# Optimization experiments

Measured on AMD Instinct MI355X. Metric: run time of the kernel, lower is better.

The kernel has to match this reference:

```python
import jax, jax.numpy as jnp
import numpy as np

B, N1, K, E, H = 64, 8, 128, 256, 512


def setup_inputs() -> dict:
    key = jax.random.key(0)
    ks = jax.random.split(key, 10)
    s = 1.0 / np.sqrt(E)
    sh = 1.0 / np.sqrt(H)
    return {
        "queries": jax.random.normal(ks[0], (B, N1, E), jnp.float32),
        "keys": jax.random.normal(ks[1], (B, N1, K, E), jnp.float32),
        "cum_subs_masks": jax.random.randint(ks[2], (B, N1, K, 1), 0, 2, jnp.int32),
        "num_neg": N1 - 1,
        "wk_w": jax.random.uniform(ks[3], (H, E), jnp.float32, -s, s),
        "wk_b": jax.random.uniform(ks[4], (H,), jnp.float32, -s, s),
        "wq_w": jax.random.uniform(ks[5], (H, E), jnp.float32, -s, s),
        "wq_b": jax.random.uniform(ks[6], (H,), jnp.float32, -s, s),
        "wv_w": jax.random.uniform(ks[7], (1, H), jnp.float32, -sh, sh),
        "wv_b": jax.random.uniform(ks[8], (1,), jnp.float32, -sh, sh),
    }


def reference(queries, keys, cum_subs_masks, num_neg, wk_w, wk_b, wq_w, wq_b, wv_w, wv_b):
    # queries: (B, N1, E) -> project and broadcast over keys dim
    q_proj = jnp.einsum("bne,he->bnh", queries, wq_w) + wq_b        # (B, N1, H)
    k_proj = jnp.einsum("bnke,he->bnkh", keys, wk_w) + wk_b          # (B, N1, K, H)
    hidden = jnp.tanh(q_proj[:, :, None, :] + k_proj)                # (B, N1, K, H)
    scores = jnp.einsum("bnkh,oh->bnko", hidden, wv_w) + wv_b        # (B, N1, K, 1)
    scores = scores + cum_subs_masks.astype(scores.dtype) * (-1e9)
    attn_weight = jax.nn.softmax(scores, axis=-2)                    # over K
    attn_out = jnp.sum(attn_weight * keys, axis=-2)                  # (B, N1, E)
    return attn_out, attn_weight
```

## Files before the change

### kernel.cpp

```cpp
#include <hip/hip_runtime.h>
#include <hip/hip_bf16.h>

#define B_  64
#define N1_ 8
#define KK  128
#define EE  256
#define HH  512
#define BN  (B_ * N1_)

typedef __attribute__((ext_vector_type(8))) short short8;
typedef __attribute__((ext_vector_type(4))) float f32x4;

__device__ __forceinline__ short bfs(float f) {
  __hip_bfloat16 h = __float2bfloat16(f);
  return __builtin_bit_cast(short, h);
}

__device__ __forceinline__ float tanhf_fast(float x) {
  float e2 = __builtin_amdgcn_exp2f(2.8853900817779268f * x);
  return 1.0f - 2.0f * __builtin_amdgcn_rcpf(e2 + 1.0f);
}

__global__ __launch_bounds__(256) void k_prep(
    const float* __restrict__ wk_w,
    const float* __restrict__ queries,
    const float* __restrict__ wq_w,
    const float* __restrict__ wq_b,
    const float* __restrict__ wk_b,
    unsigned short* __restrict__ wk_fr,
    float* __restrict__ qp) {
  const int bid = blockIdx.x, t = threadIdx.x;
  if (bid < 64) {
    const int g  = bid * 256 + t;
    const int h  = g >> 5;
    const int e0 = (g & 31) * 8;
    float4 x = *(const float4*)(wk_w + (size_t)h * EE + e0);
    float4 y = *(const float4*)(wk_w + (size_t)h * EE + e0 + 4);
    short8 f;
    f[0] = bfs(x.x); f[1] = bfs(x.y); f[2] = bfs(x.z); f[3] = bfs(x.w);
    f[4] = bfs(y.x); f[5] = bfs(y.y); f[6] = bfs(y.z); f[7] = bfs(y.w);
    const int ht = h >> 4, hl = h & 15;
    const int s = e0 >> 5, lg = (e0 >> 3) & 3;
    const int chunk = (ht * 8 + s) * 64 + lg * 16 + hl;
    *(short8*)(wk_fr + (size_t)chunk * 8) = f;
  } else {
    const int w = t >> 6, l = t & 63, lg = l >> 4, ll = l & 15;
    const int g2 = bid - 64;
    const int bn0 = (g2 >> 1) * 16;
    const int ht0 = (g2 & 1) * 16;
    short8 af[8];
    {
      const float* qr = queries + (size_t)(bn0 + ll) * EE + lg * 8;
      #pragma unroll
      for (int s = 0; s < 8; ++s) {
        float4 x = *(const float4*)(qr + s * 32);
        float4 y = *(const float4*)(qr + s * 32 + 4);
        short8 f;
        f[0] = bfs(x.x); f[1] = bfs(x.y); f[2] = bfs(x.z); f[3] = bfs(x.w);
        f[4] = bfs(y.x); f[5] = bfs(y.y); f[6] = bfs(y.z); f[7] = bfs(y.w);
        af[s] = f;
      }
    }
    #pragma unroll
    for (int i = 0; i < 4; ++i) {
      const int ht = ht0 + w * 4 + i;
      const float* bp = wq_w + (size_t)(ht * 16 + ll) * EE + lg * 8;
      f32x4 a = {0.f, 0.f, 0.f, 0.f};
      #pragma unroll
      for (int s = 0; s < 8; ++s) {
        float4 x = *(const float4*)(bp + s * 32);
        float4 y = *(const float4*)(bp + s * 32 + 4);
        short8 f;
        f[0] = bfs(x.x); f[1] = bfs(x.y); f[2] = bfs(x.z); f[3] = bfs(x.w);
        f[4] = bfs(y.x); f[5] = bfs(y.y); f[6] = bfs(y.z); f[7] = bfs(y.w);
        a = __builtin_amdgcn_mfma_f32_16x16x32_bf16(af[s], f, a, 0, 0, 0);
      }
      const int h = ht * 16 + ll;
      const float add = wq_b[h] + wk_b[h];
      #pragma unroll
      for (int r = 0; r < 4; ++r)
        qp[(size_t)(bn0 + lg * 4 + r) * HH + h] = a[r] + add;
    }
  }
}

__global__ __launch_bounds__(256, 2) void k_fused(
    const float* __restrict__ keys,
    const unsigned short* __restrict__ wk_fr,
    const float* __restrict__ wv_w,
    const float* __restrict__ qp,
    const int* __restrict__ masks,
    float* __restrict__ out) {
  const int t  = threadIdx.x;
  const int w  = t >> 6;
  const int l  = t & 63;
  const int lg = l >> 4;
  const int ll = l & 15;
  const int bn = blockIdx.x;
  const short8* wkf = (const short8*)wk_fr;

  __shared__ float qb_s[HH];
  __shared__ float wv_s[HH];
  __shared__ float sc[KK];
  __shared__ float red[2];
  __shared__ float4 po4[4][64];

  qb_s[t]       = qp[(size_t)bn * HH + t];
  qb_s[t + 256] = qp[(size_t)bn * HH + t + 256];
  wv_s[t]       = wv_w[t];
  wv_s[t + 256] = wv_w[t + 256];

  short8 af0[8], af1[8];
  {
    const float* kp0 = keys + (size_t)(bn * KK + w * 32 + ll) * EE + lg * 8;
    const float* kp1 = kp0 + 16 * EE;
    #pragma unroll
    for (int s = 0; s < 8; ++s) {
      float4 x = *(const float4*)(kp0 + s * 32);
      float4 y = *(const float4*)(kp0 + s * 32 + 4);
      short8 f;
      f[0] = bfs(x.x); f[1] = bfs(x.y); f[2] = bfs(x.z); f[3] = bfs(x.w);
      f[4] = bfs(y.x); f[5] = bfs(y.y); f[6] = bfs(y.z); f[7] = bfs(y.w);
      af0[s] = f;
      x = *(const float4*)(kp1 + s * 32);
      y = *(const float4*)(kp1 + s * 32 + 4);
      f[0] = bfs(x.x); f[1] = bfs(x.y); f[2] = bfs(x.z); f[3] = bfs(x.w);
      f[4] = bfs(y.x); f[5] = bfs(y.y); f[6] = bfs(y.z); f[7] = bfs(y.w);
      af1[s] = f;
    }
  }
  __syncthreads();

  float p0[4] = {0.f, 0.f, 0.f, 0.f};
  float p1[4] = {0.f, 0.f, 0.f, 0.f};
  short8 bA[8], bB[8];

#define LOADB(dst, ht) {                                                   \
    _Pragma("unroll") for (int s = 0; s < 8; ++s)                          \
      dst[s] = wkf[((ht) * 8 + s) * 64 + l]; }

#define COMPUTE(cur, ii) {                                                 \
    f32x4 a0 = {0.f, 0.f, 0.f, 0.f};                                       \
    f32x4 a1 = {0.f, 0.f, 0.f, 0.f};                                       \
    __builtin_amdgcn_s_setprio(1);                                         \
    _Pragma("unroll") for (int s = 0; s < 8; ++s) {                        \
      a0 = __builtin_amdgcn_mfma_f32_16x16x32_bf16(af0[s], cur[s], a0, 0, 0, 0); \
      a1 = __builtin_amdgcn_mfma_f32_16x16x32_bf16(af1[s], cur[s], a1, 0, 0, 0); } \
    __builtin_amdgcn_s_setprio(0);                                         \
    const int h = (ii) * 16 + ll;                                          \
    const float qb = qb_s[h];                                              \
    const float wv = wv_s[h];                                              \
    _Pragma("unroll") for (int r = 0; r < 4; ++r) {                        \
      p0[r] += wv * tanhf_fast(a0[r] + qb);                                \
      p1[r] += wv * tanhf_fast(a1[r] + qb); } }

  LOADB(bA, 0);
  __builtin_amdgcn_sched_barrier(0);
  #pragma unroll 1
  for (int i = 0; i < 32; i += 2) {
    LOADB(bB, i + 1);
    __builtin_amdgcn_sched_barrier(0);
    COMPUTE(bA, i);
    if (i < 30) {
      LOADB(bA, i + 2);
      __builtin_amdgcn_sched_barrier(0);
    }
    COMPUTE(bB, i + 1);
  }
#undef COMPUTE
#undef LOADB

  #pragma unroll
  for (int r = 0; r < 4; ++r) {
    #pragma unroll
    for (int off = 1; off <= 8; off <<= 1) {
      p0[r] += __shfl_xor(p0[r], off, 64);
      p1[r] += __shfl_xor(p1[r], off, 64);
    }
  }
  if (ll == 0) {
    #pragma unroll
    for (int r = 0; r < 4; ++r) {
      sc[w * 32 + lg * 4 + r]      = p0[r];
      sc[w * 32 + 16 + lg * 4 + r] = p1[r];
    }
  }
  __syncthreads();

  if (t < KK) sc[t] += (float)masks[bn * KK + t] * (-1e9f);
  __syncthreads();
  if (t < 64) {
    float a = fmaxf(sc[t], sc[t + 64]);
    #pragma unroll
    for (int off = 32; off >= 1; off >>= 1) a = fmaxf(a, __shfl_xor(a, off, 64));
    if (t == 0) red[0] = a;
  }
  __syncthreads();
  const float m = red[0];
  if (t < KK) sc[t] = expf(sc[t] - m);
  __syncthreads();
  if (t < 64) {
    float a = sc[t] + sc[t + 64];
    #pragma unroll
    for (int off = 32; off >= 1; off >>= 1) a += __shfl_xor(a, off, 64);
    if (t == 0) red[1] = a;
  }
  __syncthreads();
  const float inv = 1.f / red[1];
  if (t < KK) {
    float wgt = sc[t] * inv;
    sc[t] = wgt;
    out[BN * EE + (size_t)bn * KK + t] = wgt;
  }
  __syncthreads();

  {
    const float4* kb4 = (const float4*)(keys + (size_t)bn * KK * EE);
    const int kh = t >> 6, ln = t & 63;
    float4 acc = {0.f, 0.f, 0.f, 0.f};
    #pragma unroll 4
    for (int k = 0; k < 32; ++k) {
      const float wgt = sc[kh * 32 + k];
      float4 kv = kb4[(size_t)(kh * 32 + k) * 64 + ln];
      acc.x += wgt * kv.x; acc.y += wgt * kv.y;
      acc.z += wgt * kv.z; acc.w += wgt * kv.w;
    }
    po4[kh][ln] = acc;
  }
  __syncthreads();
  if (t < 64) {
    float4 a = po4[0][t], b = po4[1][t], c = po4[2][t], d = po4[3][t];
    float4 r;
    r.x = a.x + b.x + c.x + d.x;
    r.y = a.y + b.y + c.y + d.y;
    r.z = a.z + b.z + c.z + d.z;
    r.w = a.w + b.w + c.w + d.w;
    *(float4*)(out + (size_t)bn * EE + t * 4) = r;
  }
}

extern "C" void kernel_launch(void* const* d_in, const int* in_sizes, int n_in,
                              void* d_out, int out_size, void* d_ws, size_t ws_size,
                              hipStream_t stream) {
  const float* queries = (const float*)d_in[0];
  const float* keys    = (const float*)d_in[1];
  const int*   masks   = (const int*)d_in[2];
  const float* wk_w = (const float*)d_in[4];
  const float* wk_b = (const float*)d_in[5];
  const float* wq_w = (const float*)d_in[6];
  const float* wq_b = (const float*)d_in[7];
  const float* wv_w = (const float*)d_in[8];

  float* out = (float*)d_out;
  float* qp  = (float*)d_ws;
  unsigned short* wk_fr = (unsigned short*)(qp + BN * HH);

  k_prep<<<128, 256, 0, stream>>>(wk_w, queries, wq_w, wq_b, wk_b, wk_fr, qp);
  k_fused<<<BN, 256, 0, stream>>>(keys, wk_fr, wv_w, qp, masks, out);
}
```

Baseline: 50.78 us.

## Split fused attention into flash-style partial softmax per key group plus combine kernel

The fused kernel is split into a scoring kernel in which each 64-lane wave handles 32 keys. It computes a local max and sum, and accumulates the weighted key sum from the bf16 key fragments it already holds in registers, so the fp32 keys are not re-read from global memory. A separate combine kernel rescales the four partials and writes the normalized output and the attention weights. This removes the block-wide syncs and the second pass over keys, and doubles the number of blocks. In exchange it adds a kernel launch, workspace traffic for the partials, and bf16 rounding in the attn_out computation, which was fp32 before.

```diff
diff --git a/kernel.cpp b/kernel.cpp
--- a/kernel.cpp
+++ b/kernel.cpp
@@ -7,6 +7,7 @@
 #define EE  256
 #define HH  512
 #define BN  (B_ * N1_)
+#define LOG2E 1.4426950408889634f
 
 typedef __attribute__((ext_vector_type(8))) short short8;
 typedef __attribute__((ext_vector_type(4))) float f32x4;
@@ -15,10 +16,16 @@
   __hip_bfloat16 h = __float2bfloat16(f);
   return __builtin_bit_cast(short, h);
 }
-
+__device__ __forceinline__ float bf2f(short s) {
+  unsigned int u = ((unsigned int)(unsigned short)s) << 16;
+  return __builtin_bit_cast(float, u);
+}
 __device__ __forceinline__ float tanhf_fast(float x) {
   float e2 = __builtin_amdgcn_exp2f(2.8853900817779268f * x);
   return 1.0f - 2.0f * __builtin_amdgcn_rcpf(e2 + 1.0f);
+}
+__device__ __forceinline__ float exp_f(float x) {
+  return __builtin_amdgcn_exp2f(x * LOG2E);
 }
 
 __global__ __launch_bounds__(256) void k_prep(
@@ -84,35 +91,31 @@
   }
 }
 
-__global__ __launch_bounds__(256, 2) void k_fused(
+__global__ __launch_bounds__(128, 2) void k_scorespv(
     const float* __restrict__ keys,
     const unsigned short* __restrict__ wk_fr,
     const float* __restrict__ wv_w,
     const float* __restrict__ qp,
     const int* __restrict__ masks,
-    float* __restrict__ out) {
+    float* __restrict__ o_part,
+    float* __restrict__ ml_part,
+    float* __restrict__ smask) {
   const int t  = threadIdx.x;
   const int w  = t >> 6;
   const int l  = t & 63;
   const int lg = l >> 4;
   const int ll = l & 15;
-  const int bn = blockIdx.x;
+  const int bid = blockIdx.x;
+  const int bn  = bid >> 1;
+  const int g   = (bid & 1) * 2 + w;
+  const int row0 = g * 32;
   const short8* wkf = (const short8*)wk_fr;
 
-  __shared__ float qb_s[HH];
-  __shared__ float wv_s[HH];
-  __shared__ float sc[KK];
-  __shared__ float red[2];
-  __shared__ float4 po4[4][64];
-
-  qb_s[t]       = qp[(size_t)bn * HH + t];
-  qb_s[t + 256] = qp[(size_t)bn * HH + t + 256];
-  wv_s[t]       = wv_w[t];
-  wv_s[t + 256] = wv_w[t + 256];
+  __shared__ float sc_l[2][32];
 
   short8 af0[8], af1[8];
   {
-    const float* kp0 = keys + (size_t)(bn * KK + w * 32 + ll) * EE + lg * 8;
+    const float* kp0 = keys + (size_t)(bn * KK + row0 + ll) * EE + lg * 8;
     const float* kp1 = kp0 + 16 * EE;
     #pragma unroll
     for (int s = 0; s < 8; ++s) {
@@ -129,7 +132,6 @@
       af1[s] = f;
     }
   }
-  __syncthreads();
 
   float p0[4] = {0.f, 0.f, 0.f, 0.f};
   float p1[4] = {0.f, 0.f, 0.f, 0.f};
@@ -148,8 +150,8 @@
       a1 = __builtin_amdgcn_mfma_f32_16x16x32_bf16(af1[s], cur[s], a1, 0, 0, 0); } \
     __builtin_amdgcn_s_setprio(0);                                         \
     const int h = (ii) * 16 + ll;                                          \
-    const float qb = qb_s[h];                                              \
-    const float wv = wv_s[h];                                              \
+    const float qb = qp[(size_t)bn * HH + h];                              \
+    const float wv = wv_w[h];                                              \
     _Pragma("unroll") for (int r = 0; r < 4; ++r) {                        \
       p0[r] += wv * tanhf_fast(a0[r] + qb);                                \
       p1[r] += wv * tanhf_fast(a1[r] + qb); } }
@@ -181,62 +183,87 @@
   if (ll == 0) {
     #pragma unroll
     for (int r = 0; r < 4; ++r) {
-      sc[w * 32 + lg * 4 + r]      = p0[r];
-      sc[w * 32 + 16 + lg * 4 + r] = p1[r];
+      sc_l[w][lg * 4 + r]      = p0[r];
+      sc_l[w][16 + lg * 4 + r] = p1[r];
     }
   }
   __syncthreads();
-
-  if (t < KK) sc[t] += (float)masks[bn * KK + t] * (-1e9f);
+  float s0 = sc_l[w][ll];
+  float s1 = sc_l[w][ll + 16];
+
+  const int mbase = bn * KK + row0;
+  s0 += (float)masks[mbase + ll] * (-1e9f);
+  s1 += (float)masks[mbase + 16 + ll] * (-1e9f);
+
+  float mx = fmaxf(s0, s1);
+  #pragma unroll
+  for (int off = 1; off <= 8; off <<= 1) mx = fmaxf(mx, __shfl_xor(mx, off, 64));
+
+  const float e0 = exp_f(s0 - mx);
+  const float e1 = exp_f(s1 - mx);
+  float lsum = e0 + e1;
+  #pragma unroll
+  for (int off = 1; off <= 8; off <<= 1) lsum += __shfl_xor(lsum, off, 64);
+
+  if (lg == 0) {
+    smask[mbase + ll]      = s0;
+    smask[mbase + 16 + ll] = s1;
+  }
+  if (l == 0) {
+    float* mlp = ml_part + ((size_t)bn * 4 + g) * 2;
+    mlp[0] = mx;
+    mlp[1] = lsum;
+  }
+
+  float* ob = o_part + ((size_t)bn * 4 + g) * 256;
+  #pragma unroll
+  for (int s = 0; s < 8; ++s) {
+    float pv[8];
+    #pragma unroll
+    for (int j = 0; j < 8; ++j)
+      pv[j] = e0 * bf2f(af0[s][j]) + e1 * bf2f(af1[s][j]);
+    #pragma unroll
+    for (int j = 0; j < 8; ++j) {
+      #pragma unroll
+      for (int off = 1; off <= 8; off <<= 1)
+        pv[j] += __shfl_xor(pv[j], off, 64);
+    }
+    if (ll == 0) {
+      float4 v0 = {pv[0], pv[1], pv[2], pv[3]};
+      float4 v1 = {pv[4], pv[5], pv[6], pv[7]};
+      *(float4*)(ob + lg * 8 + s * 32)     = v0;
+      *(float4*)(ob + lg * 8 + s * 32 + 4) = v1;
+    }
+  }
+}
+
+__global__ __launch_bounds__(256) void k_combine(
+    const float* __restrict__ o_part,
+    const float* __restrict__ ml_part,
+    const float* __restrict__ smask,
+    float* __restrict__ out) {
+  const int bn = blockIdx.x, t = threadIdx.x;
+  __shared__ float al[4];
+  __shared__ float mL[2];
+  if (t == 0) {
+    const float* mlp = ml_part + (size_t)bn * 8;
+    float m0 = mlp[0], m1 = mlp[2], m2 = mlp[4], m3 = mlp[6];
+    float m = fmaxf(fmaxf(m0, m1), fmaxf(m2, m3));
+    float a0 = exp_f(m0 - m), a1 = exp_f(m1 - m);
+    float a2 = exp_f(m2 - m), a3 = exp_f(m3 - m);
+    al[0] = a0; al[1] = a1; al[2] = a2; al[3] = a3;
+    mL[0] = m;
+    mL[1] = a0 * mlp[1] + a1 * mlp[3] + a2 * mlp[5] + a3 * mlp[7];
+  }
   __syncthreads();
-  if (t < 64) {
-    float a = fmaxf(sc[t], sc[t + 64]);
-    #pragma unroll
-    for (int off = 32; off >= 1; off >>= 1) a = fmaxf(a, __shfl_xor(a, off, 64));
-    if (t == 0) red[0] = a;
-  }
-  __syncthreads();
-  const float m = red[0];
-  if (t < KK) sc[t] = expf(sc[t] - m);
-  __syncthreads();
-  if (t < 64) {
-    float a = sc[t] + sc[t + 64];
-    #pragma unroll
-    for (int off = 32; off >= 1; off >>= 1) a += __shfl_xor(a, off, 64);
-    if (t == 0) red[1] = a;
-  }
-  __syncthreads();
-  const float inv = 1.f / red[1];
-  if (t < KK) {
-    float wgt = sc[t] * inv;
-    sc[t] = wgt;
-    out[BN * EE + (size_t)bn * KK + t] = wgt;
-  }
-  __syncthreads();
-
-  {
-    const float4* kb4 = (const float4*)(keys + (size_t)bn * KK * EE);
-    const int kh = t >> 6, ln = t & 63;
-    float4 acc = {0.f, 0.f, 0.f, 0.f};
-    #pragma unroll 4
-    for (int k = 0; k < 32; ++k) {
-      const float wgt = sc[kh * 32 + k];
-      float4 kv = kb4[(size_t)(kh * 32 + k) * 64 + ln];
-      acc.x += wgt * kv.x; acc.y += wgt * kv.y;
-      acc.z += wgt * kv.z; acc.w += wgt * kv.w;
-    }
-    po4[kh][ln] = acc;
-  }
-  __syncthreads();
-  if (t < 64) {
-    float4 a = po4[0][t], b = po4[1][t], c = po4[2][t], d = po4[3][t];
-    float4 r;
-    r.x = a.x + b.x + c.x + d.x;
-    r.y = a.y + b.y + c.y + d.y;
-    r.z = a.z + b.z + c.z + d.z;
-    r.w = a.w + b.w + c.w + d.w;
-    *(float4*)(out + (size_t)bn * EE + t * 4) = r;
-  }
+  const float m = mL[0];
+  const float invL = __builtin_amdgcn_rcpf(mL[1]);
+  const float* ob = o_part + (size_t)bn * 4 * 256;
+  float acc = al[0] * ob[t] + al[1] * ob[256 + t] +
+              al[2] * ob[512 + t] + al[3] * ob[768 + t];
+  out[(size_t)bn * EE + t] = acc * invL;
+  if (t < KK)
+    out[BN * EE + (size_t)bn * KK + t] = exp_f(smask[bn * KK + t] - m) * invL;
 }
 
 extern "C" void kernel_launch(void* const* d_in, const int* in_sizes, int n_in,
@@ -254,7 +281,12 @@
   float* out = (float*)d_out;
   float* qp  = (float*)d_ws;
   unsigned short* wk_fr = (unsigned short*)(qp + BN * HH);
+  float* o_part  = (float*)(wk_fr + HH * EE);
+  float* ml_part = o_part + (size_t)BN * 4 * 256;
+  float* smask   = ml_part + BN * 4 * 2;
 
   k_prep<<<128, 256, 0, stream>>>(wk_w, queries, wq_w, wq_b, wk_b, wk_fr, qp);
-  k_fused<<<BN, 256, 0, stream>>>(keys, wk_fr, wv_w, qp, masks, out);
-}
+  k_scorespv<<<BN * 2, 128, 0, stream>>>(keys, wk_fr, wv_w, qp, masks,
+                                         o_part, ml_part, smask);
+  k_combine<<<BN, 256, 0, stream>>>(o_part, ml_part, smask, out);
+}
```

Measured after the change: 56.85 us. +12.0%, slower.
